# Kernel optimization log

Hardware: AMD Instinct MI355X
Metric: run time of the kernel (lower is better)

The kernel has to match this reference:

```python
import jax, jax.numpy as jnp
import numpy as np

D_MODEL = 1024
N_HEADS = 16
D_K = D_MODEL // N_HEADS
D_FF = 4096
B, S = 2, 2048
EPS = 1e-5
SCALE = 0.02


def setup_inputs() -> dict:
    key = jax.random.key(0)
    ks = jax.random.split(key, 8)
    return {
        "x": jax.random.normal(ks[0], (B, S, D_MODEL), dtype=jnp.float32),
        "ln1_w": jnp.ones((D_MODEL,), jnp.float32),
        "ln1_b": jnp.zeros((D_MODEL,), jnp.float32),
        "Wq": jax.random.normal(ks[1], (D_MODEL, D_MODEL), jnp.float32) * SCALE,
        "bq": jnp.zeros((D_MODEL,), jnp.float32),
        "Wk": jax.random.normal(ks[2], (D_MODEL, D_MODEL), jnp.float32) * SCALE,
        "bk": jnp.zeros((D_MODEL,), jnp.float32),
        "Wv": jax.random.normal(ks[3], (D_MODEL, D_MODEL), jnp.float32) * SCALE,
        "bv": jnp.zeros((D_MODEL,), jnp.float32),
        "Wo": jax.random.normal(ks[4], (D_MODEL, D_MODEL), jnp.float32) * SCALE,
        "bo": jnp.zeros((D_MODEL,), jnp.float32),
        "ln2_w": jnp.ones((D_MODEL,), jnp.float32),
        "ln2_b": jnp.zeros((D_MODEL,), jnp.float32),
        "W1": jax.random.normal(ks[5], (D_MODEL, D_FF), jnp.float32) * SCALE,
        "b1": jnp.zeros((D_FF,), jnp.float32),
        "W2": jax.random.normal(ks[6], (D_FF, D_MODEL), jnp.float32) * SCALE,
        "b2": jnp.zeros((D_MODEL,), jnp.float32),
    }


def _layernorm(x, w, b):
    mu = jnp.mean(x, axis=-1, keepdims=True)
    var = jnp.mean(jnp.square(x - mu), axis=-1, keepdims=True)
    return (x - mu) * jax.lax.rsqrt(var + EPS) * w + b


def reference(x, ln1_w, ln1_b, Wq, bq, Wk, bk, Wv, bv, Wo, bo,
              ln2_w, ln2_b, W1, b1, W2, b2):
    # Pre-norm multi-head self-attention (dropout = identity, eval mode)
    h = _layernorm(x, ln1_w, ln1_b)                      # [B,S,D]
    q = (h @ Wq + bq).reshape(B, S, N_HEADS, D_K)        # [B,S,H,Dk]
    k = (h @ Wk + bk).reshape(B, S, N_HEADS, D_K)
    v = (h @ Wv + bv).reshape(B, S, N_HEADS, D_K)
    scores = jnp.einsum('bqhd,bkhd->bhqk', q, k) / jnp.sqrt(jnp.float32(D_K))
    attn = jax.nn.softmax(scores, axis=-1)               # [B,H,S,S]
    ctx = jnp.einsum('bhqk,bkhd->bqhd', attn, v).reshape(B, S, D_MODEL)
    x = x + (ctx @ Wo + bo)
    # Pre-norm FFN
    h2 = _layernorm(x, ln2_w, ln2_b)
    ff = jax.nn.relu(h2 @ W1 + b1) @ W2 + b2
    return x + ff
```

## Files before the change

kernel.cpp:

```cpp
#include <hip/hip_runtime.h>
#include <hip/hip_bf16.h>
#include <cstdint>
#include <cstddef>

typedef unsigned short ushort_t;
typedef __bf16 bf16x8 __attribute__((ext_vector_type(8)));
typedef float f32x4 __attribute__((ext_vector_type(4)));
typedef float f32x16 __attribute__((ext_vector_type(16)));

#define D_MODEL 1024
#define D_FF 4096
#define BB 2
#define SS 2048
#define NH 16
#define MROWS (BB * SS)
#define KVBLK 64

__device__ __forceinline__ ushort_t f2bf(float f) {
  union { float f; unsigned u; } x; x.f = f;
  unsigned r = x.u + 0x7fffu + ((x.u >> 16) & 1u);
  return (ushort_t)(r >> 16);
}

__device__ __forceinline__ void gload_lds16(const void* g, void* l) {
  __builtin_amdgcn_global_load_lds((const __attribute__((address_space(1))) void*)g,
                                   (__attribute__((address_space(3))) void*)l, 16, 0, 0);
}

__device__ __forceinline__ bf16x8 pack4w(unsigned w0, unsigned w1, unsigned w2, unsigned w3) {
  union { unsigned u[4]; bf16x8 v; } t;
  t.u[0] = w0; t.u[1] = w1; t.u[2] = w2; t.u[3] = w3;
  return t.v;
}

__global__ __launch_bounds__(256) void ln_bf16_kernel(
    const float* __restrict__ x, const float* __restrict__ w,
    const float* __restrict__ b, ushort_t* __restrict__ out) {
  int row = blockIdx.x;
  int tid = threadIdx.x;
  int lane = tid & 63, wid = tid >> 6;
  const float4 v = ((const float4*)(x + (size_t)row * D_MODEL))[tid];
  float s = v.x + v.y + v.z + v.w;
  __shared__ float red[8];
  #pragma unroll
  for (int o = 32; o > 0; o >>= 1) s += __shfl_down(s, o);
  if (lane == 0) red[wid] = s;
  __syncthreads();
  float mu = (red[0] + red[1] + red[2] + red[3]) * (1.0f / D_MODEL);
  float d0 = v.x - mu, d1 = v.y - mu, d2 = v.z - mu, d3 = v.w - mu;
  float sq = d0 * d0 + d1 * d1 + d2 * d2 + d3 * d3;
  #pragma unroll
  for (int o = 32; o > 0; o >>= 1) sq += __shfl_down(sq, o);
  if (lane == 0) red[4 + wid] = sq;
  __syncthreads();
  float var = (red[4] + red[5] + red[6] + red[7]) * (1.0f / D_MODEL);
  float rstd = rsqrtf(var + 1e-5f);
  const float4 wv = ((const float4*)w)[tid];
  const float4 bv = ((const float4*)b)[tid];
  ushort4 o4;
  o4.x = f2bf(d0 * rstd * wv.x + bv.x);
  o4.y = f2bf(d1 * rstd * wv.y + bv.y);
  o4.z = f2bf(d2 * rstd * wv.z + bv.z);
  o4.w = f2bf(d3 * rstd * wv.w + bv.w);
  ((ushort4*)(out + (size_t)row * D_MODEL))[tid] = o4;
}

__global__ __launch_bounds__(256) void transpose_cast_kernel(
    const float* __restrict__ W, ushort_t* __restrict__ Wt, int K, int N) {
  __shared__ float tile[32][33];
  int bx = blockIdx.x * 32;
  int by = blockIdx.y * 32;
  int tx = threadIdx.x, ty = threadIdx.y;
  #pragma unroll
  for (int i = 0; i < 32; i += 8)
    tile[ty + i][tx] = W[(size_t)(by + ty + i) * N + bx + tx];
  __syncthreads();
  #pragma unroll
  for (int i = 0; i < 32; i += 8)
    Wt[(size_t)(bx + ty + i) * K + by + tx] = f2bf(tile[tx][ty + i]);
}

__global__ __launch_bounds__(256) void vtrans_kernel(
    const ushort_t* __restrict__ qkv, ushort_t* __restrict__ Vt) {
  __shared__ __align__(16) ushort_t T[64 * 64];
  const int tid = threadIdx.x;
  const int bh = blockIdx.y, b = bh >> 4, h = bh & 15;
  const int kv0 = blockIdx.x * 64;
  const ushort_t* Vp = qkv + (size_t)b * SS * 3072 + 2048 + h * 64;
  #pragma unroll
  for (int i = 0; i < 2; i++) {
    int idx = tid * 2 + i;
    int key = idx >> 3, c = idx & 7;
    bf16x8 v = *(const bf16x8*)(Vp + (size_t)(kv0 + key) * 3072 + c * 8);
    *(bf16x8*)(T + key * 64 + ((c ^ (key & 7)) * 8)) = v;
  }
  __syncthreads();
  int d = tid >> 2, kb = tid & 3;
  ushort_t o[16];
  #pragma unroll
  for (int j = 0; j < 16; j++) {
    int key = kb * 16 + j;
    o[j] = T[key * 64 + (((d >> 3) ^ (key & 7)) * 8) + (d & 7)];
  }
  ushort_t* dst = Vt + (size_t)(bh * 64 + d) * SS + kv0 + kb * 16;
  *(bf16x8*)dst = *(bf16x8*)&o[0];
  *(bf16x8*)(dst + 8) = *(bf16x8*)&o[8];
}

template <int EPI>
__global__ __launch_bounds__(256, 2) void gemm128_kernel(
    const ushort_t* __restrict__ A, const ushort_t* __restrict__ Bt,
    const float* __restrict__ bias, const float* __restrict__ resid,
    void* __restrict__ Cout, int M, int N, int K, int NTn, int Ksplit, int MTN) {
  __shared__ __align__(16) ushort_t lds[4][2][4096];
  const int tid = threadIdx.x, lane = tid & 63, wid = tid >> 6;
  const int wm = wid >> 1, wn = wid & 1;
  const int rl = lane & 15, cg = lane >> 4;
  int nwg = gridDim.x;
  int q = nwg >> 3, rr = nwg & 7;
  int xcd = blockIdx.x & 7, idx = blockIdx.x >> 3;
  int wgid = (xcd < rr ? xcd * (q + 1) : rr * (q + 1) + (xcd - rr) * q) + idx;
  const int s = wgid / MTN;
  int rem = wgid - s * MTN;
  const int row0 = (rem / NTn) * 128, col0 = (rem - (rem / NTn) * NTn) * 128;
  const int k0 = s * Ksplit;
  const int NT = Ksplit / 32;

  int soff[2], ldso[2];
  #pragma unroll
  for (int i = 0; i < 2; i++) {
    int ci = wid * 128 + i * 64 + lane;
    int P = ci * 16;
    int L = P ^ (((P >> 7) & 7) << 4);
    int row = L >> 6, kc = (L >> 4) & 3;
    soff[i] = row * K + kc * 8;
    ldso[i] = (wid * 128 + i * 64) * 8;
  }

  f32x4 acc[4][4] = {};

  auto stage = [&](int t) {
    int b = t & 3;
    int kk = k0 + t * 32;
    #pragma unroll
    for (int i = 0; i < 2; i++) {
      gload_lds16(A + (size_t)row0 * K + kk + soff[i], &lds[b][0][ldso[i]]);
      gload_lds16(Bt + (size_t)col0 * K + kk + soff[i], &lds[b][1][ldso[i]]);
    }
  };

  auto compute = [&](int t) {
    int b = t & 3;
    bf16x8 af[4], bfv[4];
    #pragma unroll
    for (int mi = 0; mi < 4; mi++) {
      int r = wm * 64 + mi * 16 + rl;
      int L = r * 64 + cg * 16;
      int P = L ^ (((L >> 7) & 7) << 4);
      af[mi] = *(const bf16x8*)&lds[b][0][P >> 1];
    }
    #pragma unroll
    for (int ni = 0; ni < 4; ni++) {
      int r = wn * 64 + ni * 16 + rl;
      int L = r * 64 + cg * 16;
      int P = L ^ (((L >> 7) & 7) << 4);
      bfv[ni] = *(const bf16x8*)&lds[b][1][P >> 1];
    }
    __builtin_amdgcn_s_setprio(1);
    #pragma unroll
    for (int mi = 0; mi < 4; mi++)
      #pragma unroll
      for (int ni = 0; ni < 4; ni++)
        acc[mi][ni] = __builtin_amdgcn_mfma_f32_16x16x32_bf16(af[mi], bfv[ni], acc[mi][ni], 0, 0, 0);
    __builtin_amdgcn_s_setprio(0);
  };

  stage(0); stage(1); stage(2);
  for (int t = 0; t < NT; ++t) {
    if (t < NT - 2)       asm volatile("s_waitcnt vmcnt(8)" ::: "memory");
    else if (t == NT - 2) asm volatile("s_waitcnt vmcnt(4)" ::: "memory");
    else                  asm volatile("s_waitcnt vmcnt(0)" ::: "memory");
    __builtin_amdgcn_s_barrier();
    __builtin_amdgcn_sched_barrier(0);
    if (t + 3 < NT) stage(t + 3);
    compute(t);
  }

  if (EPI == 2) {
    float* out = (float*)Cout;
    #pragma unroll
    for (int ni = 0; ni < 4; ni++) {
      int col = col0 + wn * 64 + ni * 16 + rl;
      float bv = bias[col];
      #pragma unroll
      for (int mi = 0; mi < 4; mi++) {
        int rowb = row0 + wm * 64 + mi * 16 + cg * 4;
        #pragma unroll
        for (int j = 0; j < 4; j++)
          out[(size_t)(rowb + j) * N + col] =
              acc[mi][ni][j] + bv + resid[(size_t)(rowb + j) * N + col];
      }
    }
  } else if (EPI == 3) {
    float* out = (float*)Cout + (size_t)s * M * N;
    #pragma unroll
    for (int ni = 0; ni < 4; ni++) {
      int col = col0 + wn * 64 + ni * 16 + rl;
      #pragma unroll
      for (int mi = 0; mi < 4; mi++) {
        int rowb = row0 + wm * 64 + mi * 16 + cg * 4;
        #pragma unroll
        for (int j = 0; j < 4; j++)
          out[(size_t)(rowb + j) * N + col] = acc[mi][ni][j];
      }
    }
  } else {
    ushort_t* out = (ushort_t*)Cout;
    #pragma unroll
    for (int ni = 0; ni < 4; ni++) {
      int col = col0 + wn * 64 + ni * 16 + rl;
      float bv = bias[col];
      float sc = (EPI == 0 && col < 1024) ? 0.18033688011f : 1.0f;
      #pragma unroll
      for (int mi = 0; mi < 4; mi++) {
        int rowb = row0 + wm * 64 + mi * 16 + cg * 4;
        #pragma unroll
        for (int j = 0; j < 4; j++) {
          float v = acc[mi][ni][j] + bv;
          if (EPI == 1) v = fmaxf(v, 0.0f);
          if (EPI == 0) v *= sc;
          out[(size_t)(rowb + j) * N + col] = f2bf(v);
        }
      }
    }
  }
}

__global__ __launch_bounds__(256) void reduce_kernel(
    const float* __restrict__ p, const float* __restrict__ bias,
    const float* __restrict__ resid, float* __restrict__ out,
    int S, size_t total4, size_t stride4) {
  const float4* p4 = (const float4*)p;
  const float4* r4 = (const float4*)resid;
  const float4* b4 = (const float4*)bias;
  float4* o4 = (float4*)out;
  for (size_t i = (size_t)blockIdx.x * 256 + threadIdx.x; i < total4;
       i += (size_t)gridDim.x * 256) {
    float4 a = r4[i];
    float4 bb = b4[i & 255];
    a.x += bb.x; a.y += bb.y; a.z += bb.z; a.w += bb.w;
    for (int s = 0; s < S; ++s) {
      float4 v = p4[(size_t)s * stride4 + i];
      a.x += v.x; a.y += v.y; a.z += v.z; a.w += v.w;
    }
    o4[i] = a;
  }
}

__global__ __launch_bounds__(256) void attn_kernel(
    const ushort_t* __restrict__ qkv, const ushort_t* __restrict__ Vt,
    ushort_t* __restrict__ ctx) {
  __shared__ __align__(16) ushort_t Kl[2][64 * 64];
  __shared__ __align__(16) ushort_t Vl[2][64 * 64];
  __shared__ float Lt[4][32];
  const int tid = threadIdx.x, lane = tid & 63, wid = tid >> 6;
  int bid = blockIdx.y * 16 + blockIdx.x;
  int w = (bid & 7) * 64 + (bid >> 3);
  const int bh = w >> 4, qt = w & 15;
  const int b = bh >> 4, h = bh & 15;
  const int q0w = qt * 128 + wid * 32;
  const int k31 = lane & 31, sg = lane >> 5, x7 = k31 & 7;
  const ushort_t* Qp = qkv + (size_t)b * SS * 3072 + h * 64;
  const ushort_t* Kp = Qp + 1024;
  const ushort_t* Vg = Vt + (size_t)bh * 64 * SS;

  bf16x8 qf[4];
  {
    const ushort_t* qb = Qp + (size_t)(q0w + k31) * 3072 + sg * 8;
    #pragma unroll
    for (int dsl = 0; dsl < 4; dsl++)
      qf[dsl] = *(const bf16x8*)(qb + dsl * 16);
  }
  float lsum = 0.f;
  f32x16 o0 = {}, o1 = {};

  const int NT = SS / KVBLK;

  int ksrc[2], vsrc[2];
  #pragma unroll
  for (int i = 0; i < 2; i++) {
    int idx = wid * 128 + i * 64 + lane;
    int R = idx >> 3, c = idx & 7;
    ksrc[i] = R * 3072 + ((c ^ (R & 7)) * 8);
    vsrc[i] = R * SS + ((c ^ (R & 7)) * 8);
  }
  const int ldsb = wid * 1024;

  auto stageKV = [&](int buf, int t) {
    size_t kvK = (size_t)t * KVBLK * 3072;
    int kvV = t * KVBLK;
    gload_lds16(Kp + kvK + ksrc[0], &Kl[buf][ldsb]);
    gload_lds16(Kp + kvK + ksrc[1], &Kl[buf][ldsb + 512]);
    gload_lds16(Vg + kvV + vsrc[0], &Vl[buf][ldsb]);
    gload_lds16(Vg + kvV + vsrc[1], &Vl[buf][ldsb + 512]);
  };

  auto softmax_half = [&](const f32x16& s, bf16x8& paE, bf16x8& paO) {
    float pv[16];
    #pragma unroll
    for (int r = 0; r < 16; r++) pv[r] = __builtin_amdgcn_exp2f(s[r]);
    #pragma unroll
    for (int r = 0; r < 16; r++) lsum += pv[r];
    unsigned W[4][2];
    #pragma unroll
    for (int qd = 0; qd < 4; qd++) {
      asm("v_cvt_pk_bf16_f32 %0, %1, %2" : "=v"(W[qd][0]) : "v"(pv[4 * qd]), "v"(pv[4 * qd + 1]));
      asm("v_cvt_pk_bf16_f32 %0, %1, %2" : "=v"(W[qd][1]) : "v"(pv[4 * qd + 2]), "v"(pv[4 * qd + 3]));
    }
    unsigned a0 = W[1][0], b0 = W[0][0], a1 = W[1][1], b1 = W[0][1];
    asm("v_permlane32_swap_b32 %0, %1" : "+v"(a0), "+v"(b0));
    asm("v_permlane32_swap_b32 %0, %1" : "+v"(a1), "+v"(b1));
    paE = pack4w(b0, b1, a0, a1);
    unsigned a2 = W[3][0], b2 = W[2][0], a3 = W[3][1], b3 = W[2][1];
    asm("v_permlane32_swap_b32 %0, %1" : "+v"(a2), "+v"(b2));
    asm("v_permlane32_swap_b32 %0, %1" : "+v"(a3), "+v"(b3));
    paO = pack4w(b2, b3, a2, a3);
  };

  auto body = [&](int t, int cb) {
    __syncthreads();
    if (t + 1 < NT) stageKV(cb ^ 1, t + 1);

    f32x16 s0 = {}, s1 = {};
    #pragma unroll
    for (int dsl = 0; dsl < 4; dsl++) {
      int ch = ((dsl * 2 + sg) ^ x7) * 8;
      bf16x8 kf0 = *(const bf16x8*)(&Kl[cb][k31 * 64 + ch]);
      bf16x8 kf1 = *(const bf16x8*)(&Kl[cb][(32 + k31) * 64 + ch]);
      s0 = __builtin_amdgcn_mfma_f32_32x32x16_bf16(kf0, qf[dsl], s0, 0, 0, 0);
      s1 = __builtin_amdgcn_mfma_f32_32x32x16_bf16(kf1, qf[dsl], s1, 0, 0, 0);
    }
    bf16x8 pa[4];
    softmax_half(s0, pa[0], pa[1]);
    softmax_half(s1, pa[2], pa[3]);
    #pragma unroll
    for (int ks = 0; ks < 4; ks++) {
      int ch = ((2 * ks + sg) ^ x7) * 8;
      bf16x8 vf0 = *(const bf16x8*)(&Vl[cb][k31 * 64 + ch]);
      bf16x8 vf1 = *(const bf16x8*)(&Vl[cb][(32 + k31) * 64 + ch]);
      o0 = __builtin_amdgcn_mfma_f32_32x32x16_bf16(pa[ks], vf0, o0, 0, 0, 0);
      o1 = __builtin_amdgcn_mfma_f32_32x32x16_bf16(pa[ks], vf1, o1, 0, 0, 0);
    }
  };

  stageKV(0, 0);
  for (int t = 0; t < NT; t += 2) {
    body(t, 0);
    body(t + 1, 1);
  }

  float ltot = lsum + __shfl_xor(lsum, 32);
  if (lane < 32) Lt[wid][lane] = ltot;
  asm volatile("s_waitcnt lgkmcnt(0)" ::: "memory");
  __builtin_amdgcn_sched_barrier(0);

  const int colb = h * 64 + k31;
  #pragma unroll
  for (int r = 0; r < 16; r++) {
    int qp = (r & 3) + 8 * (r >> 2) + 4 * sg;
    float rlq = 1.0f / Lt[wid][qp];
    size_t row = (size_t)(b * SS + q0w + qp);
    ctx[row * D_MODEL + colb] = f2bf(o0[r] * rlq);
    ctx[row * D_MODEL + colb + 32] = f2bf(o1[r] * rlq);
  }
}

extern "C" void kernel_launch(void* const* d_in, const int* in_sizes, int n_in,
                              void* d_out, int out_size, void* d_ws, size_t ws_size,
                              hipStream_t stream) {
  const float* x    = (const float*)d_in[0];
  const float* ln1w = (const float*)d_in[1];
  const float* ln1b = (const float*)d_in[2];
  const float* Wq   = (const float*)d_in[3];
  const float* bq   = (const float*)d_in[4];
  const float* Wk   = (const float*)d_in[5];
  const float* bk   = (const float*)d_in[6];
  const float* Wv   = (const float*)d_in[7];
  const float* bv   = (const float*)d_in[8];
  const float* Wo   = (const float*)d_in[9];
  const float* bo   = (const float*)d_in[10];
  const float* ln2w = (const float*)d_in[11];
  const float* ln2b = (const float*)d_in[12];
  const float* W1   = (const float*)d_in[13];
  const float* b1   = (const float*)d_in[14];
  const float* W2   = (const float*)d_in[15];
  const float* b2   = (const float*)d_in[16];

  char* ws = (char*)d_ws;
  size_t off = 0;
  auto alloc = [&](size_t bytes) {
    void* p = ws + off;
    off += (bytes + 255) & ~(size_t)255;
    return p;
  };
  ushort_t* Wt_qkv = (ushort_t*)alloc((size_t)3072 * 1024 * 2);
  ushort_t* Wt_o   = (ushort_t*)alloc((size_t)1024 * 1024 * 2);
  ushort_t* Wt_1   = (ushort_t*)alloc((size_t)4096 * 1024 * 2);
  ushort_t* Wt_2   = (ushort_t*)alloc((size_t)1024 * 4096 * 2);
  float*    bqkv   = (float*)alloc((size_t)3072 * 4);
  ushort_t* qkvb   = (ushort_t*)alloc((size_t)MROWS * 3072 * 2);
  ushort_t* ctxb   = (ushort_t*)alloc((size_t)MROWS * 1024 * 2);
  ushort_t* hbuf   = (ushort_t*)alloc((size_t)MROWS * 1024 * 2);
  float*    x2     = (float*)alloc((size_t)MROWS * 1024 * 4);
  ushort_t* Vtb    = (ushort_t*)alloc((size_t)BB * NH * 64 * SS * 2);
  ushort_t* ff1    = qkvb;
  float*    outp   = (float*)d_out;

  const size_t partial1 = (size_t)MROWS * 1024 * 4;
  int S = (ws_size - off >= 2 * partial1 + 256) ? 2 : 1;
  float* pbuf = (S == 2) ? (float*)alloc(2 * partial1) : nullptr;

  dim3 tb(32, 8);
  transpose_cast_kernel<<<dim3(32, 32), tb, 0, stream>>>(Wq, Wt_qkv, 1024, 1024);
  transpose_cast_kernel<<<dim3(32, 32), tb, 0, stream>>>(Wk, Wt_qkv + 1024 * 1024, 1024, 1024);
  transpose_cast_kernel<<<dim3(32, 32), tb, 0, stream>>>(Wv, Wt_qkv + 2 * 1024 * 1024, 1024, 1024);
  transpose_cast_kernel<<<dim3(32, 32), tb, 0, stream>>>(Wo, Wt_o, 1024, 1024);
  transpose_cast_kernel<<<dim3(128, 32), tb, 0, stream>>>(W1, Wt_1, 1024, 4096);
  transpose_cast_kernel<<<dim3(32, 128), tb, 0, stream>>>(W2, Wt_2, 4096, 1024);
  hipMemcpyAsync(bqkv,        bq, 1024 * 4, hipMemcpyDeviceToDevice, stream);
  hipMemcpyAsync(bqkv + 1024, bk, 1024 * 4, hipMemcpyDeviceToDevice, stream);
  hipMemcpyAsync(bqkv + 2048, bv, 1024 * 4, hipMemcpyDeviceToDevice, stream);

  ln_bf16_kernel<<<MROWS, 256, 0, stream>>>(x, ln1w, ln1b, hbuf);
  gemm128_kernel<0><<<dim3(24 * 32), 256, 0, stream>>>(
      hbuf, Wt_qkv, bqkv, nullptr, qkvb, MROWS, 3072, 1024, 24, 1024, 24 * 32);
  vtrans_kernel<<<dim3(SS / 64, BB * NH), 256, 0, stream>>>(qkvb, Vtb);
  attn_kernel<<<dim3(SS / 128, BB * NH), 256, 0, stream>>>(qkvb, Vtb, ctxb);
  gemm128_kernel<2><<<dim3(8 * 32), 256, 0, stream>>>(
      ctxb, Wt_o, bo, x, x2, MROWS, 1024, 1024, 8, 1024, 8 * 32);
  ln_bf16_kernel<<<MROWS, 256, 0, stream>>>(x2, ln2w, ln2b, hbuf);
  gemm128_kernel<1><<<dim3(32 * 32), 256, 0, stream>>>(
      hbuf, Wt_1, b1, nullptr, ff1, MROWS, D_FF, 1024, 32, 1024, 32 * 32);
  if (S == 2) {
    gemm128_kernel<3><<<dim3(8 * 32 * 2), 256, 0, stream>>>(
        ff1, Wt_2, nullptr, nullptr, pbuf, MROWS, 1024, 4096, 8, 2048, 8 * 32);
    reduce_kernel<<<2048, 256, 0, stream>>>(pbuf, b2, x2, outp, 2,
        (size_t)MROWS * 1024 / 4, (size_t)MROWS * 1024 / 4);
  } else {
    gemm128_kernel<2><<<dim3(8 * 32), 256, 0, stream>>>(
        ff1, Wt_2, b2, x2, outp, MROWS, 1024, 4096, 8, 4096, 8 * 32);
  }
}
```

Before: 246.1 us.

## Double attention KV tile and batch weight transposes and bias packing into fewer launches

Attention now stages 128 keys per iteration instead of 64. The V tile is re-laid out with a 16-way XOR swizzle, and four score MFMAs plus eight PV MFMAs run per step, halving the number of barriers and stage rounds. The four 1024x1024 weight transposes are merged into one launch using a z-grid. The three bias memcpys are replaced by a single pack kernel. This trades twice the LDS per block (more shared memory, possibly lower occupancy) for fewer syncs and fewer kernel and copy launches.

```diff
diff --git a/kernel.cpp b/kernel.cpp
--- a/kernel.cpp
+++ b/kernel.cpp
@@ -14,7 +14,7 @@
 #define SS 2048
 #define NH 16
 #define MROWS (BB * SS)
-#define KVBLK 64
+#define KVBLK 128
 
 __device__ __forceinline__ ushort_t f2bf(float f) {
   union { float f; unsigned u; } x; x.f = f;
@@ -78,6 +78,34 @@
   #pragma unroll
   for (int i = 0; i < 32; i += 8)
     Wt[(size_t)(bx + ty + i) * K + by + tx] = f2bf(tile[tx][ty + i]);
+}
+
+__global__ __launch_bounds__(256) void transpose_cast4_kernel(
+    const float* __restrict__ Wq, const float* __restrict__ Wk,
+    const float* __restrict__ Wv, const float* __restrict__ Wo,
+    ushort_t* __restrict__ Dqkv, ushort_t* __restrict__ Do_) {
+  __shared__ float tile[32][33];
+  int z = blockIdx.z;
+  const float* W = (z == 0) ? Wq : (z == 1) ? Wk : (z == 2) ? Wv : Wo;
+  ushort_t* Wt = (z < 3) ? (Dqkv + (size_t)z * 1024 * 1024) : Do_;
+  int bx = blockIdx.x * 32;
+  int by = blockIdx.y * 32;
+  int tx = threadIdx.x, ty = threadIdx.y;
+  #pragma unroll
+  for (int i = 0; i < 32; i += 8)
+    tile[ty + i][tx] = W[(size_t)(by + ty + i) * 1024 + bx + tx];
+  __syncthreads();
+  #pragma unroll
+  for (int i = 0; i < 32; i += 8)
+    Wt[(size_t)(bx + ty + i) * 1024 + by + tx] = f2bf(tile[tx][ty + i]);
+}
+
+__global__ __launch_bounds__(256) void biaspack_kernel(
+    const float* __restrict__ bq, const float* __restrict__ bk,
+    const float* __restrict__ bv, float* __restrict__ out) {
+  int i = blockIdx.x * 256 + threadIdx.x;
+  float v = (i < 1024) ? bq[i] : (i < 2048) ? bk[i - 1024] : bv[i - 2048];
+  out[i] = v;
 }
 
 __global__ __launch_bounds__(256) void vtrans_kernel(
@@ -260,8 +288,8 @@
 __global__ __launch_bounds__(256) void attn_kernel(
     const ushort_t* __restrict__ qkv, const ushort_t* __restrict__ Vt,
     ushort_t* __restrict__ ctx) {
-  __shared__ __align__(16) ushort_t Kl[2][64 * 64];
-  __shared__ __align__(16) ushort_t Vl[2][64 * 64];
+  __shared__ __align__(16) ushort_t Kl[2][128 * 64];
+  __shared__ __align__(16) ushort_t Vl[2][64 * 128];
   __shared__ float Lt[4][32];
   const int tid = threadIdx.x, lane = tid & 63, wid = tid >> 6;
   int bid = blockIdx.y * 16 + blockIdx.x;
@@ -269,7 +297,7 @@
   const int bh = w >> 4, qt = w & 15;
   const int b = bh >> 4, h = bh & 15;
   const int q0w = qt * 128 + wid * 32;
-  const int k31 = lane & 31, sg = lane >> 5, x7 = k31 & 7;
+  const int k31 = lane & 31, sg = lane >> 5, x7 = k31 & 7, x15 = k31 & 15;
   const ushort_t* Qp = qkv + (size_t)b * SS * 3072 + h * 64;
   const ushort_t* Kp = Qp + 1024;
   const ushort_t* Vg = Vt + (size_t)bh * 64 * SS;
@@ -286,23 +314,24 @@
 
   const int NT = SS / KVBLK;
 
-  int ksrc[2], vsrc[2];
-  #pragma unroll
-  for (int i = 0; i < 2; i++) {
-    int idx = wid * 128 + i * 64 + lane;
-    int R = idx >> 3, c = idx & 7;
-    ksrc[i] = R * 3072 + ((c ^ (R & 7)) * 8);
-    vsrc[i] = R * SS + ((c ^ (R & 7)) * 8);
-  }
-  const int ldsb = wid * 1024;
+  int ksrc[4], vsrc[4];
+  #pragma unroll
+  for (int i = 0; i < 4; i++) {
+    int idx = wid * 256 + i * 64 + lane;
+    { int R = idx >> 3, c = idx & 7;  ksrc[i] = R * 3072 + ((c ^ (R & 7)) * 8); }
+    { int R = idx >> 4, c = idx & 15; vsrc[i] = R * SS + ((c ^ (R & 15)) * 8); }
+  }
+  const int ldsb = wid * 2048;
 
   auto stageKV = [&](int buf, int t) {
     size_t kvK = (size_t)t * KVBLK * 3072;
     int kvV = t * KVBLK;
-    gload_lds16(Kp + kvK + ksrc[0], &Kl[buf][ldsb]);
-    gload_lds16(Kp + kvK + ksrc[1], &Kl[buf][ldsb + 512]);
-    gload_lds16(Vg + kvV + vsrc[0], &Vl[buf][ldsb]);
-    gload_lds16(Vg + kvV + vsrc[1], &Vl[buf][ldsb + 512]);
+    #pragma unroll
+    for (int i = 0; i < 4; i++)
+      gload_lds16(Kp + kvK + ksrc[i], &Kl[buf][ldsb + i * 512]);
+    #pragma unroll
+    for (int i = 0; i < 4; i++)
+      gload_lds16(Vg + kvV + vsrc[i], &Vl[buf][ldsb + i * 512]);
   };
 
   auto softmax_half = [&](const f32x16& s, bf16x8& paE, bf16x8& paO) {
@@ -331,23 +360,29 @@
     __syncthreads();
     if (t + 1 < NT) stageKV(cb ^ 1, t + 1);
 
-    f32x16 s0 = {}, s1 = {};
+    f32x16 s0 = {}, s1 = {}, s2 = {}, s3 = {};
     #pragma unroll
     for (int dsl = 0; dsl < 4; dsl++) {
       int ch = ((dsl * 2 + sg) ^ x7) * 8;
-      bf16x8 kf0 = *(const bf16x8*)(&Kl[cb][k31 * 64 + ch]);
+      bf16x8 kf0 = *(const bf16x8*)(&Kl[cb][(k31) * 64 + ch]);
       bf16x8 kf1 = *(const bf16x8*)(&Kl[cb][(32 + k31) * 64 + ch]);
+      bf16x8 kf2 = *(const bf16x8*)(&Kl[cb][(64 + k31) * 64 + ch]);
+      bf16x8 kf3 = *(const bf16x8*)(&Kl[cb][(96 + k31) * 64 + ch]);
       s0 = __builtin_amdgcn_mfma_f32_32x32x16_bf16(kf0, qf[dsl], s0, 0, 0, 0);
       s1 = __builtin_amdgcn_mfma_f32_32x32x16_bf16(kf1, qf[dsl], s1, 0, 0, 0);
-    }
-    bf16x8 pa[4];
+      s2 = __builtin_amdgcn_mfma_f32_32x32x16_bf16(kf2, qf[dsl], s2, 0, 0, 0);
+      s3 = __builtin_amdgcn_mfma_f32_32x32x16_bf16(kf3, qf[dsl], s3, 0, 0, 0);
+    }
+    bf16x8 pa[8];
     softmax_half(s0, pa[0], pa[1]);
     softmax_half(s1, pa[2], pa[3]);
-    #pragma unroll
-    for (int ks = 0; ks < 4; ks++) {
-      int ch = ((2 * ks + sg) ^ x7) * 8;
-      bf16x8 vf0 = *(const bf16x8*)(&Vl[cb][k31 * 64 + ch]);
-      bf16x8 vf1 = *(const bf16x8*)(&Vl[cb][(32 + k31) * 64 + ch]);
+    softmax_half(s2, pa[4], pa[5]);
+    softmax_half(s3, pa[6], pa[7]);
+    #pragma unroll
+    for (int ks = 0; ks < 8; ks++) {
+      int chv = ((2 * ks + sg) ^ x15) * 8;
+      bf16x8 vf0 = *(const bf16x8*)(&Vl[cb][(k31) * 128 + chv]);
+      bf16x8 vf1 = *(const bf16x8*)(&Vl[cb][(32 + k31) * 128 + chv]);
       o0 = __builtin_amdgcn_mfma_f32_32x32x16_bf16(pa[ks], vf0, o0, 0, 0, 0);
       o1 = __builtin_amdgcn_mfma_f32_32x32x16_bf16(pa[ks], vf1, o1, 0, 0, 0);
     }
@@ -421,15 +456,10 @@
   float* pbuf = (S == 2) ? (float*)alloc(2 * partial1) : nullptr;
 
   dim3 tb(32, 8);
-  transpose_cast_kernel<<<dim3(32, 32), tb, 0, stream>>>(Wq, Wt_qkv, 1024, 1024);
-  transpose_cast_kernel<<<dim3(32, 32), tb, 0, stream>>>(Wk, Wt_qkv + 1024 * 1024, 1024, 1024);
-  transpose_cast_kernel<<<dim3(32, 32), tb, 0, stream>>>(Wv, Wt_qkv + 2 * 1024 * 1024, 1024, 1024);
-  transpose_cast_kernel<<<dim3(32, 32), tb, 0, stream>>>(Wo, Wt_o, 1024, 1024);
+  transpose_cast4_kernel<<<dim3(32, 32, 4), tb, 0, stream>>>(Wq, Wk, Wv, Wo, Wt_qkv, Wt_o);
   transpose_cast_kernel<<<dim3(128, 32), tb, 0, stream>>>(W1, Wt_1, 1024, 4096);
   transpose_cast_kernel<<<dim3(32, 128), tb, 0, stream>>>(W2, Wt_2, 4096, 1024);
-  hipMemcpyAsync(bqkv,        bq, 1024 * 4, hipMemcpyDeviceToDevice, stream);
-  hipMemcpyAsync(bqkv + 1024, bk, 1024 * 4, hipMemcpyDeviceToDevice, stream);
-  hipMemcpyAsync(bqkv + 2048, bv, 1024 * 4, hipMemcpyDeviceToDevice, stream);
+  biaspack_kernel<<<12, 256, 0, stream>>>(bq, bk, bv, bqkv);
 
   ln_bf16_kernel<<<MROWS, 256, 0, stream>>>(x, ln1w, ln1b, hbuf);
   gemm128_kernel<0><<<dim3(24 * 32), 256, 0, stream>>>(
```

Result: slower. 256.9 us (+4.4%).

## Shrink GEMM LDS ring to 3 stages for 3 waves/SIMD, merge prologue launches

Applied to the files above, without the earlier changes.

The GEMM's LDS pipeline drops from a 4-buffer ring prefetching 3 tiles ahead to a 3-buffer ring prefetching 2 ahead. This cuts shared memory per block from 64 KB to 48 KB, and launch bounds are raised so three blocks can be resident per CU. The four square weight transpose-casts are merged into one launch, and the three bias memcpys become one small kernel, to cut launch overhead. The trade-off is a shallower prefetch, which gives less latency hiding per block and may add register pressure from the higher occupancy target.

```diff
diff --git a/kernel.cpp b/kernel.cpp
--- a/kernel.cpp
+++ b/kernel.cpp
@@ -80,6 +80,34 @@
     Wt[(size_t)(bx + ty + i) * K + by + tx] = f2bf(tile[tx][ty + i]);
 }
 
+__global__ __launch_bounds__(256) void transpose_cast4_kernel(
+    const float* __restrict__ Wq, const float* __restrict__ Wk,
+    const float* __restrict__ Wv, const float* __restrict__ Wo,
+    ushort_t* __restrict__ Dqkv, ushort_t* __restrict__ Do_) {
+  __shared__ float tile[32][33];
+  int z = blockIdx.z;
+  const float* W = (z == 0) ? Wq : (z == 1) ? Wk : (z == 2) ? Wv : Wo;
+  ushort_t* Wt = (z < 3) ? (Dqkv + (size_t)z * 1024 * 1024) : Do_;
+  int bx = blockIdx.x * 32;
+  int by = blockIdx.y * 32;
+  int tx = threadIdx.x, ty = threadIdx.y;
+  #pragma unroll
+  for (int i = 0; i < 32; i += 8)
+    tile[ty + i][tx] = W[(size_t)(by + ty + i) * 1024 + bx + tx];
+  __syncthreads();
+  #pragma unroll
+  for (int i = 0; i < 32; i += 8)
+    Wt[(size_t)(bx + ty + i) * 1024 + by + tx] = f2bf(tile[tx][ty + i]);
+}
+
+__global__ __launch_bounds__(256) void biaspack_kernel(
+    const float* __restrict__ bq, const float* __restrict__ bk,
+    const float* __restrict__ bv, float* __restrict__ out) {
+  int i = blockIdx.x * 256 + threadIdx.x;
+  float v = (i < 1024) ? bq[i] : (i < 2048) ? bk[i - 1024] : bv[i - 2048];
+  out[i] = v;
+}
+
 __global__ __launch_bounds__(256) void vtrans_kernel(
     const ushort_t* __restrict__ qkv, ushort_t* __restrict__ Vt) {
   __shared__ __align__(16) ushort_t T[64 * 64];
@@ -108,11 +136,11 @@
 }
 
 template <int EPI>
-__global__ __launch_bounds__(256, 2) void gemm128_kernel(
+__global__ __launch_bounds__(256, 3) void gemm128_kernel(
     const ushort_t* __restrict__ A, const ushort_t* __restrict__ Bt,
     const float* __restrict__ bias, const float* __restrict__ resid,
     void* __restrict__ Cout, int M, int N, int K, int NTn, int Ksplit, int MTN) {
-  __shared__ __align__(16) ushort_t lds[4][2][4096];
+  __shared__ __align__(16) ushort_t lds[3][2][4096];
   const int tid = threadIdx.x, lane = tid & 63, wid = tid >> 6;
   const int wm = wid >> 1, wn = wid & 1;
   const int rl = lane & 15, cg = lane >> 4;
@@ -139,8 +167,7 @@
 
   f32x4 acc[4][4] = {};
 
-  auto stage = [&](int t) {
-    int b = t & 3;
+  auto stage = [&](int t, int b) {
     int kk = k0 + t * 32;
     #pragma unroll
     for (int i = 0; i < 2; i++) {
@@ -149,8 +176,7 @@
     }
   };
 
-  auto compute = [&](int t) {
-    int b = t & 3;
+  auto compute = [&](int b) {
     bf16x8 af[4], bfv[4];
     #pragma unroll
     for (int mi = 0; mi < 4; mi++) {
@@ -175,15 +201,16 @@
     __builtin_amdgcn_s_setprio(0);
   };
 
-  stage(0); stage(1); stage(2);
+  stage(0, 0); stage(1, 1);
+  int sb = 2, cb = 0;
   for (int t = 0; t < NT; ++t) {
-    if (t < NT - 2)       asm volatile("s_waitcnt vmcnt(8)" ::: "memory");
-    else if (t == NT - 2) asm volatile("s_waitcnt vmcnt(4)" ::: "memory");
-    else                  asm volatile("s_waitcnt vmcnt(0)" ::: "memory");
+    if (t < NT - 1) asm volatile("s_waitcnt vmcnt(4)" ::: "memory");
+    else            asm volatile("s_waitcnt vmcnt(0)" ::: "memory");
     __builtin_amdgcn_s_barrier();
     __builtin_amdgcn_sched_barrier(0);
-    if (t + 3 < NT) stage(t + 3);
-    compute(t);
+    if (t + 2 < NT) { stage(t + 2, sb); sb = (sb == 2) ? 0 : sb + 1; }
+    compute(cb);
+    cb = (cb == 2) ? 0 : cb + 1;
   }
 
   if (EPI == 2) {
@@ -421,15 +448,10 @@
   float* pbuf = (S == 2) ? (float*)alloc(2 * partial1) : nullptr;
 
   dim3 tb(32, 8);
-  transpose_cast_kernel<<<dim3(32, 32), tb, 0, stream>>>(Wq, Wt_qkv, 1024, 1024);
-  transpose_cast_kernel<<<dim3(32, 32), tb, 0, stream>>>(Wk, Wt_qkv + 1024 * 1024, 1024, 1024);
-  transpose_cast_kernel<<<dim3(32, 32), tb, 0, stream>>>(Wv, Wt_qkv + 2 * 1024 * 1024, 1024, 1024);
-  transpose_cast_kernel<<<dim3(32, 32), tb, 0, stream>>>(Wo, Wt_o, 1024, 1024);
+  transpose_cast4_kernel<<<dim3(32, 32, 4), tb, 0, stream>>>(Wq, Wk, Wv, Wo, Wt_qkv, Wt_o);
   transpose_cast_kernel<<<dim3(128, 32), tb, 0, stream>>>(W1, Wt_1, 1024, 4096);
   transpose_cast_kernel<<<dim3(32, 128), tb, 0, stream>>>(W2, Wt_2, 4096, 1024);
-  hipMemcpyAsync(bqkv,        bq, 1024 * 4, hipMemcpyDeviceToDevice, stream);
-  hipMemcpyAsync(bqkv + 1024, bk, 1024 * 4, hipMemcpyDeviceToDevice, stream);
-  hipMemcpyAsync(bqkv + 2048, bv, 1024 * 4, hipMemcpyDeviceToDevice, stream);
+  biaspack_kernel<<<12, 256, 0, stream>>>(bq, bk, bv, bqkv);
 
   ln_bf16_kernel<<<MROWS, 256, 0, stream>>>(x, ln1w, ln1b, hbuf);
   gemm128_kernel<0><<<dim3(24 * 32), 256, 0, stream>>>(
```

New measurement: 234.9 us. 4.6% less time.
